# Optimization experiments

Hardware: AMD Instinct MI355X
Metric: run time of the kernel (lower is better)

The kernel has to match this reference:

```python
import jax, jax.numpy as jnp
import numpy as np

DIM = 1024
HEADS = 16
DIM_HEAD = 64
DIM_INNER = HEADS * DIM_HEAD
SCALE = DIM_HEAD ** -0.5


def rmsnorm(x, w):
    eps = jnp.asarray(jnp.finfo(x.dtype).eps, x.dtype)
    var = jnp.mean(jnp.square(x), axis=-1, keepdims=True)
    return x * jax.lax.rsqrt(var + eps) * w


def setup_inputs() -> dict:
    key = jax.random.key(0)
    ks = jax.random.split(key, 6)
    tokens = jax.random.normal(ks[0], (2, 2048, DIM), dtype=jnp.float32)
    norm_w = jnp.ones((DIM,), dtype=jnp.float32)
    Wq = jax.random.normal(ks[1], (DIM, DIM_INNER), dtype=jnp.float32) * 0.02
    Wkv = jax.random.normal(ks[2], (DIM, 2 * DIM_INNER), dtype=jnp.float32) * 0.02
    Wout = jax.random.normal(ks[3], (DIM_INNER, DIM), dtype=jnp.float32) * 0.02
    Wg = jax.random.normal(ks[4], (DIM, HEADS), dtype=jnp.float32) * 0.02
    return {"tokens": tokens, "norm_w": norm_w, "Wq": Wq, "Wkv": Wkv, "Wout": Wout, "Wg": Wg}


def reference(tokens, norm_w, Wq, Wkv, Wout, Wg):
    b, n, _ = tokens.shape
    x = rmsnorm(tokens, norm_w)                      # [b, n, dim]
    q = x @ Wq                                       # [b, n, h*d]
    kv = x @ Wkv                                     # self-attention: context = tokens
    k, v = jnp.split(kv, 2, axis=-1)

    def split_heads(t):
        return t.reshape(b, n, HEADS, DIM_HEAD).transpose(0, 2, 1, 3)  # [b, h, n, d]

    q, k, v = map(split_heads, (q, k, v))

    sim = jnp.einsum('bhid,bhjd->bhij', q, k) * SCALE  # [b, h, n, n]
    causal_mask = jnp.triu(jnp.ones((n, n), dtype=bool), k=1)
    sim = jnp.where(causal_mask, jnp.asarray(-jnp.finfo(sim.dtype).max, sim.dtype), sim)
    attn = jax.nn.softmax(sim, axis=-1)
    out = jnp.einsum('bhij,bhjd->bhid', attn, v)       # [b, h, n, d]

    gates = jax.nn.sigmoid(x @ Wg)                     # [b, n, h]
    gates = gates.transpose(0, 2, 1)[..., None]        # [b, h, n, 1]
    out = gates * out

    out = out.transpose(0, 2, 1, 3).reshape(b, n, DIM_INNER)  # merge heads
    return out @ Wout                                  # [b, n, dim]
```

## Files before the change

kernel.cpp:

```cpp
#include <hip/hip_runtime.h>
#include <hip/hip_bf16.h>
#include <math.h>

constexpr int BB = 2;
constexpr int NN = 2048;
constexpr int DM = 1024;
constexpr int NH = 16;
constexpr int HD = 64;
constexpr int DI = NH * HD;
constexpr int MT = BB * NN;
constexpr float SM_SCALE = 0.125f * 1.44269504089f;

typedef __attribute__((ext_vector_type(8))) short short8v;
typedef __attribute__((ext_vector_type(4))) float f32x4;

__device__ inline unsigned cvt_pk_bf16(float lo, float hi) {
  unsigned r;
  asm("v_cvt_pk_bf16_f32 %0, %1, %2" : "=v"(r) : "v"(lo), "v"(hi));
  return r;
}
__device__ inline void pl32_swap(unsigned& a, unsigned& b) {
  asm("v_permlane32_swap_b32 %0, %1" : "+v"(a), "+v"(b));
}
__device__ inline void pl16_swap(unsigned& a, unsigned& b) {
  asm("v_permlane16_swap_b32 %0, %1" : "+v"(a), "+v"(b));
}
__device__ __forceinline__ void gload16(const void* g, void* l) {
  __builtin_amdgcn_global_load_lds(
      (const __attribute__((address_space(1))) unsigned int*)g,
      (__attribute__((address_space(3))) unsigned int*)l, 16, 0, 0);
}

__global__ __launch_bounds__(256) void k_rmsnorm(const float* __restrict__ tokens,
                                                 const float* __restrict__ w,
                                                 const float* __restrict__ Wg,
                                                 float* __restrict__ x,
                                                 __hip_bfloat16* __restrict__ xb,
                                                 float* __restrict__ g) {
  __shared__ float xs[DM];
  __shared__ float red[4];
  __shared__ float gred[4][16];
  const int tok = blockIdx.x;
  const int t = threadIdx.x;
  float4 v = ((const float4*)(tokens + (size_t)tok * DM))[t];
  float ss = v.x * v.x + v.y * v.y + v.z * v.z + v.w * v.w;
#pragma unroll
  for (int m = 1; m < 64; m <<= 1) ss += __shfl_xor(ss, m, 64);
  if ((t & 63) == 0) red[t >> 6] = ss;
  __syncthreads();
  float tot = red[0] + red[1] + red[2] + red[3];
  float inv = rsqrtf(tot * (1.0f / DM) + 1.1920929e-7f);
  float4 wv = ((const float4*)w)[t];
  float4 o;
  o.x = v.x * inv * wv.x;
  o.y = v.y * inv * wv.y;
  o.z = v.z * inv * wv.z;
  o.w = v.w * inv * wv.w;
  ((float4*)(x + (size_t)tok * DM))[t] = o;
  uint2 pk = make_uint2(cvt_pk_bf16(o.x, o.y), cvt_pk_bf16(o.z, o.w));
  *(uint2*)(xb + (size_t)tok * DM + t * 4) = pk;
  *(float4*)&xs[t * 4] = o;
  __syncthreads();
  const int h = t & 15, seg = t >> 4, wid = t >> 6;
  const float* xp = &xs[seg * 64];
  const float* wp = Wg + (size_t)(seg * 64) * NH + h;
  float s = 0.f;
#pragma unroll 8
  for (int k = 0; k < 64; k++) s = fmaf(xp[k], wp[(size_t)k * NH], s);
  s += __shfl_xor(s, 16);
  s += __shfl_xor(s, 32);
  if ((t & 63) < 16) gred[wid][h] = s;
  __syncthreads();
  if (t < 16) {
    float tot2 = gred[0][t] + gred[1][t] + gred[2][t] + gred[3][t];
    g[(size_t)tok * NH + t] = 1.f / (1.f + __expf(-tot2));
  }
}

__global__ __launch_bounds__(256) void k_wtrans_all(const float* __restrict__ Wq,
                                                    const float* __restrict__ Wkv,
                                                    const float* __restrict__ Wout,
                                                    __hip_bfloat16* __restrict__ Wqkvt,
                                                    __hip_bfloat16* __restrict__ Woutt) {
  const int bx = blockIdx.x;
  const int kb = blockIdx.y * 32;
  const float* W;
  __hip_bfloat16* dst;
  int N, col0, drow0;
  if (bx < 32) {
    W = Wq; N = DI; col0 = bx * 32; dst = Wqkvt; drow0 = col0;
  } else if (bx < 96) {
    W = Wkv; N = 2 * DI; col0 = (bx - 32) * 32; dst = Wqkvt; drow0 = DI + col0;
  } else {
    W = Wout; N = DM; col0 = (bx - 96) * 32; dst = Woutt; drow0 = col0;
  }
  __shared__ float tile[32][33];
  const int t = threadIdx.x;
  const int c = t & 31, r8 = t >> 5;
#pragma unroll
  for (int i = 0; i < 4; i++)
    tile[r8 + i * 8][c] = W[(size_t)(kb + r8 + i * 8) * N + col0 + c];
  __syncthreads();
#pragma unroll
  for (int i = 0; i < 4; i++)
    dst[(size_t)(drow0 + r8 + i * 8) * DM + kb + c] = __float2bfloat16(tile[c][r8 + i * 8]);
}

template <int MODE>
__global__ __launch_bounds__(256) void k_mgemm(const __hip_bfloat16* __restrict__ A,
                                               const __hip_bfloat16* __restrict__ Bt,
                                               float* __restrict__ C,
                                               __hip_bfloat16* __restrict__ OQ,
                                               __hip_bfloat16* __restrict__ OK,
                                               __hip_bfloat16* __restrict__ OV, int Nc) {
  __shared__ __hip_bfloat16 As[128][32];
  __shared__ __hip_bfloat16 Bs[64][32];
  const int t = threadIdx.x, wid = t >> 6, lane = t & 63;
  const int lq = lane & 15, lg = lane >> 4;
  const int wr = wid >> 1, wc = wid & 1;
  const int m0 = blockIdx.y * 128, n0 = blockIdx.x * 64;
  const int srow = lane >> 2, scol = (lane & 3) * 8;

  const __hip_bfloat16* Ag = A + (size_t)(m0 + wid * 32 + srow) * DM + scol;
  const __hip_bfloat16* Bg = Bt + (size_t)(n0 + wid * 16 + srow) * DM + scol;

  f32x4 acc[4][2];
#pragma unroll
  for (int i = 0; i < 4; i++)
#pragma unroll
    for (int j = 0; j < 2; j++) acc[i][j] = (f32x4){0.f, 0.f, 0.f, 0.f};

  for (int k0 = 0; k0 < DM; k0 += 32) {
    __syncthreads();
    gload16(Ag + k0, &As[wid * 32][0]);
    gload16(Ag + 16 * DM + k0, &As[wid * 32 + 16][0]);
    gload16(Bg + k0, &Bs[wid * 16][0]);
    __syncthreads();
    short8v af[4], bf[2];
#pragma unroll
    for (int i = 0; i < 4; i++) af[i] = *(const short8v*)&As[wr * 64 + i * 16 + lq][lg * 8];
#pragma unroll
    for (int j = 0; j < 2; j++) bf[j] = *(const short8v*)&Bs[wc * 32 + j * 16 + lq][lg * 8];
#pragma unroll
    for (int i = 0; i < 4; i++)
#pragma unroll
      for (int j = 0; j < 2; j++)
        acc[i][j] = __builtin_amdgcn_mfma_f32_16x16x32_bf16(af[i], bf[j], acc[i][j], 0, 0, 0);
  }

#pragma unroll
  for (int i = 0; i < 4; i++) {
    const int mb = m0 + wr * 64 + i * 16 + lg * 4;
#pragma unroll
    for (int j = 0; j < 2; j++) {
      const int c = n0 + wc * 32 + j * 16 + lq;
      if (MODE == 0) {
#pragma unroll
        for (int r = 0; r < 4; r++) C[(size_t)(mb + r) * Nc + c] = acc[i][j][r];
      } else {
        const int b = mb >> 11, nl = mb & (NN - 1);
        if (c < DI) {
          const int h = c >> 6, d = c & 63;
          __hip_bfloat16* dst = OQ + ((size_t)(b * NH + h) * NN + nl) * HD + d;
#pragma unroll
          for (int r = 0; r < 4; r++) dst[(size_t)r * HD] = __float2bfloat16(acc[i][j][r]);
        } else if (c < 2 * DI) {
          const int ck = c - DI;
          const int h = ck >> 6, d = ck & 63;
          __hip_bfloat16* dst = OK + ((size_t)(b * NH + h) * NN + nl) * HD + d;
#pragma unroll
          for (int r = 0; r < 4; r++) dst[(size_t)r * HD] = __float2bfloat16(acc[i][j][r]);
        } else {
          const int cd = c - 2 * DI;
          const int h = cd >> 6, d = cd & 63;
          uint2 pk = make_uint2(cvt_pk_bf16(acc[i][j][0], acc[i][j][1]),
                                cvt_pk_bf16(acc[i][j][2], acc[i][j][3]));
          *(uint2*)(OV + ((size_t)(b * NH + h) * HD + d) * NN + nl) = pk;
        }
      }
    }
  }
}

__global__ __launch_bounds__(64) void k_attn_mfma(const __hip_bfloat16* __restrict__ Qb,
                                                  const __hip_bfloat16* __restrict__ Kb,
                                                  const __hip_bfloat16* __restrict__ Vtb,
                                                  const float* __restrict__ gates,
                                                  __hip_bfloat16* __restrict__ aob,
                                                  float* __restrict__ Opart,
                                                  float* __restrict__ mpart,
                                                  float* __restrict__ lpart) {
  const int bid = blockIdx.x;
  const int xcd = bid & 7;
  const int s = bid >> 3;
  const int gq = s / 96;
  const int t = s % 96;
  const int bh = gq * 8 + xcd;
  const int i = t / 3, j = t % 3;
  int grp, kt0, kt1, chunk;
  if (j < 2) {
    grp = 63 - i;
    chunk = j;
    const int nt = (grp >> 1) + 1;
    const int h0 = (nt + 1) >> 1;
    kt0 = chunk ? h0 : 0;
    kt1 = chunk ? nt : h0;
  } else {
    grp = 31 - i;
    chunk = -1;
    kt0 = 0;
    kt1 = (grp >> 1) + 1;
  }
  const int lane = threadIdx.x;
  const int lg = lane >> 4, lq = lane & 15;
  const int q0 = grp * 32;

  const __hip_bfloat16* Qh = Qb + (size_t)bh * NN * HD;
  const __hip_bfloat16* Kh = Kb + (size_t)bh * NN * HD;
  const __hip_bfloat16* Vh = Vtb + (size_t)bh * HD * NN;

  short8v qf0[2], qf1[2];
#pragma unroll
  for (int ks = 0; ks < 2; ks++) {
    qf0[ks] = *(const short8v*)(Qh + (size_t)(q0 + lq) * HD + ks * 32 + lg * 8);
    qf1[ks] = *(const short8v*)(Qh + (size_t)(q0 + 16 + lq) * HD + ks * 32 + lg * 8);
  }

  f32x4 oacc0[4], oacc1[4];
#pragma unroll
  for (int jx = 0; jx < 4; jx++) {
    oacc0[jx] = (f32x4){0.f, 0.f, 0.f, 0.f};
    oacc1[jx] = (f32x4){0.f, 0.f, 0.f, 0.f};
  }
  float m0r = -3.0e38f, l0p = 0.f, m1r = -3.0e38f, l1p = 0.f;

  auto LOADK = [&](short8v (*kf)[2], int kt) {
    const int kvb = kt * 64;
#pragma unroll
    for (int jx = 0; jx < 4; jx++)
#pragma unroll
      for (int ks = 0; ks < 2; ks++)
        kf[jx][ks] = *(const short8v*)(Kh + (size_t)(kvb + jx * 16 + lq) * HD + ks * 32 + lg * 8);
  };
  auto LOADV = [&](short8v (*vf)[2], int kt) {
    const int kvb = kt * 64;
#pragma unroll
    for (int jx = 0; jx < 4; jx++)
#pragma unroll
      for (int ks = 0; ks < 2; ks++)
        vf[jx][ks] = *(const short8v*)(Vh + (size_t)(jx * 16 + lq) * NN + kvb + ks * 32 + lg * 8);
  };

  auto GROUP = [&](const short8v* qf, f32x4* oacc, float& m_run, float& l_part,
                   int q0g, const short8v (*kf)[2], const short8v (*vf)[2], int kt) {
    const int kvb = kt * 64;
    f32x4 sacc[4];
#pragma unroll
    for (int jx = 0; jx < 4; jx++) sacc[jx] = (f32x4){0.f, 0.f, 0.f, 0.f};
#pragma unroll
    for (int jx = 0; jx < 4; jx++)
#pragma unroll
      for (int ks = 0; ks < 2; ks++)
        sacc[jx] = __builtin_amdgcn_mfma_f32_16x16x32_bf16(kf[jx][ks], qf[ks], sacc[jx], 0, 0, 0);

    const int qg = q0g + lq;
    const bool diag = (kvb + 63 > q0g);
    float ss[4][4];
#pragma unroll
    for (int jx = 0; jx < 4; jx++)
#pragma unroll
      for (int r = 0; r < 4; r++) {
        float v = sacc[jx][r] * SM_SCALE;
        if (diag && (kvb + jx * 16 + lg * 4 + r > qg)) v = -3.0e38f;
        ss[jx][r] = v;
      }

    float tmax = -3.0e38f;
#pragma unroll
    for (int jx = 0; jx < 4; jx++)
#pragma unroll
      for (int r = 0; r < 4; r++) tmax = fmaxf(tmax, ss[jx][r]);

    if (!__all(tmax <= m_run + 8.0f)) {
      float tr = fmaxf(tmax, __shfl_xor(tmax, 16));
      tr = fmaxf(tr, __shfl_xor(tr, 32));
      const float mnew = fmaxf(m_run, tr);
      const float cf = exp2f(m_run - mnew);
      l_part *= cf;
#pragma unroll
      for (int jx = 0; jx < 4; jx++)
#pragma unroll
        for (int r = 0; r < 4; r++) oacc[jx][r] *= cf;
      m_run = mnew;
    }

    float psum = 0.f;
    unsigned upk[4], vpk[4];
#pragma unroll
    for (int jx = 0; jx < 4; jx++) {
      float p0 = exp2f(ss[jx][0] - m_run), p1 = exp2f(ss[jx][1] - m_run);
      float p2 = exp2f(ss[jx][2] - m_run), p3 = exp2f(ss[jx][3] - m_run);
      psum += (p0 + p1) + (p2 + p3);
      upk[jx] = cvt_pk_bf16(p0, p1);
      vpk[jx] = cvt_pk_bf16(p2, p3);
    }
    l_part += psum;

#pragma unroll
    for (int ks = 0; ks < 2; ks++) {
      unsigned w0 = upk[2 * ks], w2 = upk[2 * ks + 1];
      unsigned w1 = vpk[2 * ks], w3 = vpk[2 * ks + 1];
      pl32_swap(w0, w2);
      pl16_swap(w0, w2);
      pl32_swap(w1, w3);
      pl16_swap(w1, w3);
      int4 bw = make_int4((int)w0, (int)w1, (int)w2, (int)w3);
      short8v pb = __builtin_bit_cast(short8v, bw);
#pragma unroll
      for (int jx = 0; jx < 4; jx++)
        oacc[jx] = __builtin_amdgcn_mfma_f32_16x16x32_bf16(vf[jx][ks], pb, oacc[jx], 0, 0, 0);
    }
  };

  short8v kf[4][2], vf[4][2];
  for (int kt = kt0; kt < kt1; kt++) {
    LOADK(kf, kt);
    LOADV(vf, kt);
    GROUP(qf0, oacc0, m0r, l0p, q0, kf, vf, kt);
    GROUP(qf1, oacc1, m1r, l1p, q0 + 16, kf, vf, kt);
  }

  float l0 = l0p + __shfl_xor(l0p, 16);
  l0 += __shfl_xor(l0, 32);
  float l1 = l1p + __shfl_xor(l1p, 16);
  l1 += __shfl_xor(l1, 32);

  if (chunk >= 0) {
    const int gi = grp - 32;
    const size_t pidx = (size_t)(bh * 32 + gi) * 2 + chunk;
    float* Op = Opart + pidx * 2048;
#pragma unroll
    for (int jx = 0; jx < 4; jx++) {
      *(f32x4*)(Op + lq * 64 + jx * 16 + lg * 4) = oacc0[jx];
      *(f32x4*)(Op + (16 + lq) * 64 + jx * 16 + lg * 4) = oacc1[jx];
    }
    if (lane < 16) {
      mpart[pidx * 32 + lane] = m0r;
      mpart[pidx * 32 + 16 + lane] = m1r;
      lpart[pidx * 32 + lane] = l0;
      lpart[pidx * 32 + 16 + lane] = l1;
    }
    return;
  }

  const int b = bh >> 4, h = bh & 15;
  const float g0 = gates[((size_t)(b * NN + q0 + lq)) * NH + h];
  const float g1 = gates[((size_t)(b * NN + q0 + 16 + lq)) * NH + h];
  const float sc0 = g0 / l0, sc1 = g1 / l1;
  __shared__ float ots[32][68];
#pragma unroll
  for (int jx = 0; jx < 4; jx++)
#pragma unroll
    for (int r = 0; r < 4; r++) {
      ots[lq][jx * 16 + lg * 4 + r] = oacc0[jx][r] * sc0;
      ots[16 + lq][jx * 16 + lg * 4 + r] = oacc1[jx][r] * sc1;
    }
  __syncthreads();
  const int d0 = (lane & 3) * 16;
#pragma unroll
  for (int rr = 0; rr < 2; rr++) {
    const int rl = rr * 16 + (lane >> 2);
    __hip_bfloat16* aor = aob + ((size_t)(b * NN + q0 + rl)) * DI + h * HD + d0;
#pragma unroll
    for (int u = 0; u < 4; u++) {
      uint2 pk = make_uint2(
          cvt_pk_bf16(ots[rl][d0 + 4 * u + 0], ots[rl][d0 + 4 * u + 1]),
          cvt_pk_bf16(ots[rl][d0 + 4 * u + 2], ots[rl][d0 + 4 * u + 3]));
      *(uint2*)(aor + 4 * u) = pk;
    }
  }
}

__global__ __launch_bounds__(256) void k_attn_combine(const float* __restrict__ Opart,
                                                      const float* __restrict__ mpart,
                                                      const float* __restrict__ lpart,
                                                      const float* __restrict__ gates,
                                                      __hip_bfloat16* __restrict__ aob) {
  const int hg = blockIdx.x;
  const int h = hg >> 5, gi = hg & 31;
  const int grp = 32 + gi;
  const int t = threadIdx.x;
  const int row = t >> 3, dq = (t & 7) * 8;
  const size_t p0 = (size_t)hg * 2, p1 = p0 + 1;
  const float m0 = mpart[p0 * 32 + row], m1 = mpart[p1 * 32 + row];
  const float l0 = lpart[p0 * 32 + row], l1 = lpart[p1 * 32 + row];
  const float M = fmaxf(m0, m1);
  const float a0 = exp2f(m0 - M), a1 = exp2f(m1 - M);
  const float L = a0 * l0 + a1 * l1;
  const int b = h >> 4, hh = h & 15;
  const int grow = grp * 32 + row;
  const float sc = gates[((size_t)(b * NN + grow)) * NH + hh] / L;
  const float* O0 = Opart + p0 * 2048 + row * 64 + dq;
  const float* O1 = Opart + p1 * 2048 + row * 64 + dq;
  unsigned pk[4];
#pragma unroll
  for (int u = 0; u < 4; u++) {
    float x0 = (a0 * O0[2 * u + 0] + a1 * O1[2 * u + 0]) * sc;
    float x1 = (a0 * O0[2 * u + 1] + a1 * O1[2 * u + 1]) * sc;
    pk[u] = cvt_pk_bf16(x0, x1);
  }
  __hip_bfloat16* dst = aob + ((size_t)(b * NN + grow)) * DI + hh * 64 + dq;
  *(uint4*)dst = make_uint4(pk[0], pk[1], pk[2], pk[3]);
}

extern "C" void kernel_launch(void* const* d_in, const int* in_sizes, int n_in,
                              void* d_out, int out_size, void* d_ws, size_t ws_size,
                              hipStream_t stream) {
  const float* tokens = (const float*)d_in[0];
  const float* norm_w = (const float*)d_in[1];
  const float* Wq     = (const float*)d_in[2];
  const float* Wkv    = (const float*)d_in[3];
  const float* Wout   = (const float*)d_in[4];
  const float* Wg     = (const float*)d_in[5];
  float* out = (float*)d_out;

  float* ws = (float*)d_ws;
  float* x  = ws;
  float* gb = x + (size_t)MT * DM;
  __hip_bfloat16* xb    = (__hip_bfloat16*)(gb + (size_t)MT * NH);
  __hip_bfloat16* aob   = xb + (size_t)MT * DM;
  __hip_bfloat16* Qb    = aob + (size_t)MT * DM;
  __hip_bfloat16* Kb    = Qb + (size_t)MT * DI;
  __hip_bfloat16* Vtb   = Kb + (size_t)MT * DI;
  __hip_bfloat16* Wqkvt = Vtb + (size_t)MT * DI;
  __hip_bfloat16* Woutt = Wqkvt + (size_t)3 * DI * DM;
  float* Opart = (float*)(Woutt + (size_t)DM * DI);
  float* mpart = Opart + (size_t)2048 * 2048;
  float* lpart = mpart + (size_t)2048 * 32;

  k_rmsnorm<<<MT, 256, 0, stream>>>(tokens, norm_w, Wg, x, xb, gb);
  k_wtrans_all<<<dim3(128, 32), 256, 0, stream>>>(Wq, Wkv, Wout, Wqkvt, Woutt);
  k_mgemm<3><<<dim3(3 * DI / 64, MT / 128), 256, 0, stream>>>(
      xb, Wqkvt, nullptr, Qb, Kb, Vtb, 3 * DI);
  k_attn_mfma<<<dim3(32 * 96), 64, 0, stream>>>(Qb, Kb, Vtb, gb, aob, Opart, mpart, lpart);
  k_attn_combine<<<dim3(1024), 256, 0, stream>>>(Opart, mpart, lpart, gb, aob);
  k_mgemm<0><<<dim3(DM / 64, MT / 128), 256, 0, stream>>>(
      aob, Woutt, out, nullptr, nullptr, nullptr, DM);
}
```

Measured before the change: 176.3 us.

## Process 64 query rows per attention wave to reuse K/V loads, drop fp32 x write

The attention kernel now handles four 16-row query groups (64 rows) per single-wave block instead of two, so each K/V tile loaded into registers serves twice as many query rows. The grid is halved, split-chunk indexing and the partial-output layout are resized to match, and the combine kernel is adapted to 64-row groups. Separately, the unused fp32 normalized activation write is removed from the rmsnorm kernel. The cost is more registers per wave (extra accumulators and Q fragments) and fewer blocks, which lowers occupancy and parallelism.

```diff
diff --git a/kernel.cpp b/kernel.cpp
--- a/kernel.cpp
+++ b/kernel.cpp
@@ -34,7 +34,6 @@
 __global__ __launch_bounds__(256) void k_rmsnorm(const float* __restrict__ tokens,
                                                  const float* __restrict__ w,
                                                  const float* __restrict__ Wg,
-                                                 float* __restrict__ x,
                                                  __hip_bfloat16* __restrict__ xb,
                                                  float* __restrict__ g) {
   __shared__ float xs[DM];
@@ -56,7 +55,6 @@
   o.y = v.y * inv * wv.y;
   o.z = v.z * inv * wv.z;
   o.w = v.w * inv * wv.w;
-  ((float4*)(x + (size_t)tok * DM))[t] = o;
   uint2 pk = make_uint2(cvt_pk_bf16(o.x, o.y), cvt_pk_bf16(o.z, o.w));
   *(uint2*)(xb + (size_t)tok * DM + t * 4) = pk;
   *(float4*)&xs[t * 4] = o;
@@ -193,46 +191,51 @@
   const int bid = blockIdx.x;
   const int xcd = bid & 7;
   const int s = bid >> 3;
-  const int gq = s / 96;
-  const int t = s % 96;
+  const int gq = s / 48;
+  const int t = s % 48;
   const int bh = gq * 8 + xcd;
   const int i = t / 3, j = t % 3;
   int grp, kt0, kt1, chunk;
   if (j < 2) {
-    grp = 63 - i;
+    grp = 31 - i;
     chunk = j;
-    const int nt = (grp >> 1) + 1;
+    const int nt = grp + 1;
     const int h0 = (nt + 1) >> 1;
     kt0 = chunk ? h0 : 0;
     kt1 = chunk ? nt : h0;
   } else {
-    grp = 31 - i;
+    grp = 15 - i;
     chunk = -1;
     kt0 = 0;
-    kt1 = (grp >> 1) + 1;
+    kt1 = grp + 1;
   }
   const int lane = threadIdx.x;
   const int lg = lane >> 4, lq = lane & 15;
-  const int q0 = grp * 32;
+  const int q0 = grp * 64;
 
   const __hip_bfloat16* Qh = Qb + (size_t)bh * NN * HD;
   const __hip_bfloat16* Kh = Kb + (size_t)bh * NN * HD;
   const __hip_bfloat16* Vh = Vtb + (size_t)bh * HD * NN;
 
-  short8v qf0[2], qf1[2];
+  short8v qf0[2], qf1[2], qf2[2], qf3[2];
 #pragma unroll
   for (int ks = 0; ks < 2; ks++) {
     qf0[ks] = *(const short8v*)(Qh + (size_t)(q0 + lq) * HD + ks * 32 + lg * 8);
     qf1[ks] = *(const short8v*)(Qh + (size_t)(q0 + 16 + lq) * HD + ks * 32 + lg * 8);
-  }
-
-  f32x4 oacc0[4], oacc1[4];
+    qf2[ks] = *(const short8v*)(Qh + (size_t)(q0 + 32 + lq) * HD + ks * 32 + lg * 8);
+    qf3[ks] = *(const short8v*)(Qh + (size_t)(q0 + 48 + lq) * HD + ks * 32 + lg * 8);
+  }
+
+  f32x4 oacc0[4], oacc1[4], oacc2[4], oacc3[4];
 #pragma unroll
   for (int jx = 0; jx < 4; jx++) {
     oacc0[jx] = (f32x4){0.f, 0.f, 0.f, 0.f};
     oacc1[jx] = (f32x4){0.f, 0.f, 0.f, 0.f};
+    oacc2[jx] = (f32x4){0.f, 0.f, 0.f, 0.f};
+    oacc3[jx] = (f32x4){0.f, 0.f, 0.f, 0.f};
   }
   float m0r = -3.0e38f, l0p = 0.f, m1r = -3.0e38f, l1p = 0.f;
+  float m2r = -3.0e38f, l2p = 0.f, m3r = -3.0e38f, l3p = 0.f;
 
   auto LOADK = [&](short8v (*kf)[2], int kt) {
     const int kvb = kt * 64;
@@ -328,27 +331,35 @@
     LOADV(vf, kt);
     GROUP(qf0, oacc0, m0r, l0p, q0, kf, vf, kt);
     GROUP(qf1, oacc1, m1r, l1p, q0 + 16, kf, vf, kt);
-  }
-
-  float l0 = l0p + __shfl_xor(l0p, 16);
-  l0 += __shfl_xor(l0, 32);
-  float l1 = l1p + __shfl_xor(l1p, 16);
-  l1 += __shfl_xor(l1, 32);
+    GROUP(qf2, oacc2, m2r, l2p, q0 + 32, kf, vf, kt);
+    GROUP(qf3, oacc3, m3r, l3p, q0 + 48, kf, vf, kt);
+  }
+
+  float l0 = l0p + __shfl_xor(l0p, 16); l0 += __shfl_xor(l0, 32);
+  float l1 = l1p + __shfl_xor(l1p, 16); l1 += __shfl_xor(l1, 32);
+  float l2 = l2p + __shfl_xor(l2p, 16); l2 += __shfl_xor(l2, 32);
+  float l3 = l3p + __shfl_xor(l3p, 16); l3 += __shfl_xor(l3, 32);
 
   if (chunk >= 0) {
-    const int gi = grp - 32;
-    const size_t pidx = (size_t)(bh * 32 + gi) * 2 + chunk;
-    float* Op = Opart + pidx * 2048;
+    const int gi = grp - 16;
+    const size_t pidx = (size_t)(bh * 16 + gi) * 2 + chunk;
+    float* Op = Opart + pidx * 4096;
 #pragma unroll
     for (int jx = 0; jx < 4; jx++) {
       *(f32x4*)(Op + lq * 64 + jx * 16 + lg * 4) = oacc0[jx];
       *(f32x4*)(Op + (16 + lq) * 64 + jx * 16 + lg * 4) = oacc1[jx];
+      *(f32x4*)(Op + (32 + lq) * 64 + jx * 16 + lg * 4) = oacc2[jx];
+      *(f32x4*)(Op + (48 + lq) * 64 + jx * 16 + lg * 4) = oacc3[jx];
     }
     if (lane < 16) {
-      mpart[pidx * 32 + lane] = m0r;
-      mpart[pidx * 32 + 16 + lane] = m1r;
-      lpart[pidx * 32 + lane] = l0;
-      lpart[pidx * 32 + 16 + lane] = l1;
+      mpart[pidx * 64 + lane] = m0r;
+      mpart[pidx * 64 + 16 + lane] = m1r;
+      mpart[pidx * 64 + 32 + lane] = m2r;
+      mpart[pidx * 64 + 48 + lane] = m3r;
+      lpart[pidx * 64 + lane] = l0;
+      lpart[pidx * 64 + 16 + lane] = l1;
+      lpart[pidx * 64 + 32 + lane] = l2;
+      lpart[pidx * 64 + 48 + lane] = l3;
     }
     return;
   }
@@ -356,19 +367,23 @@
   const int b = bh >> 4, h = bh & 15;
   const float g0 = gates[((size_t)(b * NN + q0 + lq)) * NH + h];
   const float g1 = gates[((size_t)(b * NN + q0 + 16 + lq)) * NH + h];
-  const float sc0 = g0 / l0, sc1 = g1 / l1;
-  __shared__ float ots[32][68];
+  const float g2 = gates[((size_t)(b * NN + q0 + 32 + lq)) * NH + h];
+  const float g3 = gates[((size_t)(b * NN + q0 + 48 + lq)) * NH + h];
+  const float sc0 = g0 / l0, sc1 = g1 / l1, sc2 = g2 / l2, sc3 = g3 / l3;
+  __shared__ float ots[64][68];
 #pragma unroll
   for (int jx = 0; jx < 4; jx++)
 #pragma unroll
     for (int r = 0; r < 4; r++) {
       ots[lq][jx * 16 + lg * 4 + r] = oacc0[jx][r] * sc0;
       ots[16 + lq][jx * 16 + lg * 4 + r] = oacc1[jx][r] * sc1;
+      ots[32 + lq][jx * 16 + lg * 4 + r] = oacc2[jx][r] * sc2;
+      ots[48 + lq][jx * 16 + lg * 4 + r] = oacc3[jx][r] * sc3;
     }
   __syncthreads();
   const int d0 = (lane & 3) * 16;
 #pragma unroll
-  for (int rr = 0; rr < 2; rr++) {
+  for (int rr = 0; rr < 4; rr++) {
     const int rl = rr * 16 + (lane >> 2);
     __hip_bfloat16* aor = aob + ((size_t)(b * NN + q0 + rl)) * DI + h * HD + d0;
 #pragma unroll
@@ -387,30 +402,31 @@
                                                       const float* __restrict__ gates,
                                                       __hip_bfloat16* __restrict__ aob) {
   const int hg = blockIdx.x;
-  const int h = hg >> 5, gi = hg & 31;
-  const int grp = 32 + gi;
+  const int h = hg >> 4, gi = hg & 15;
+  const int grp = 16 + gi;
   const int t = threadIdx.x;
-  const int row = t >> 3, dq = (t & 7) * 8;
+  const int row = t >> 2, d0 = (t & 3) * 16;
   const size_t p0 = (size_t)hg * 2, p1 = p0 + 1;
-  const float m0 = mpart[p0 * 32 + row], m1 = mpart[p1 * 32 + row];
-  const float l0 = lpart[p0 * 32 + row], l1 = lpart[p1 * 32 + row];
+  const float m0 = mpart[p0 * 64 + row], m1 = mpart[p1 * 64 + row];
+  const float l0 = lpart[p0 * 64 + row], l1 = lpart[p1 * 64 + row];
   const float M = fmaxf(m0, m1);
   const float a0 = exp2f(m0 - M), a1 = exp2f(m1 - M);
   const float L = a0 * l0 + a1 * l1;
   const int b = h >> 4, hh = h & 15;
-  const int grow = grp * 32 + row;
+  const int grow = grp * 64 + row;
   const float sc = gates[((size_t)(b * NN + grow)) * NH + hh] / L;
-  const float* O0 = Opart + p0 * 2048 + row * 64 + dq;
-  const float* O1 = Opart + p1 * 2048 + row * 64 + dq;
-  unsigned pk[4];
-#pragma unroll
-  for (int u = 0; u < 4; u++) {
+  const float* O0 = Opart + p0 * 4096 + row * 64 + d0;
+  const float* O1 = Opart + p1 * 4096 + row * 64 + d0;
+  __hip_bfloat16* dst = aob + ((size_t)(b * NN + grow)) * DI + hh * 64 + d0;
+  unsigned pk[8];
+#pragma unroll
+  for (int u = 0; u < 8; u++) {
     float x0 = (a0 * O0[2 * u + 0] + a1 * O1[2 * u + 0]) * sc;
     float x1 = (a0 * O0[2 * u + 1] + a1 * O1[2 * u + 1]) * sc;
     pk[u] = cvt_pk_bf16(x0, x1);
   }
-  __hip_bfloat16* dst = aob + ((size_t)(b * NN + grow)) * DI + hh * 64 + dq;
   *(uint4*)dst = make_uint4(pk[0], pk[1], pk[2], pk[3]);
+  *(uint4*)(dst + 8) = make_uint4(pk[4], pk[5], pk[6], pk[7]);
 }
 
 extern "C" void kernel_launch(void* const* d_in, const int* in_sizes, int n_in,
@@ -425,8 +441,7 @@
   float* out = (float*)d_out;
 
   float* ws = (float*)d_ws;
-  float* x  = ws;
-  float* gb = x + (size_t)MT * DM;
+  float* gb = ws;
   __hip_bfloat16* xb    = (__hip_bfloat16*)(gb + (size_t)MT * NH);
   __hip_bfloat16* aob   = xb + (size_t)MT * DM;
   __hip_bfloat16* Qb    = aob + (size_t)MT * DM;
@@ -435,15 +450,15 @@
   __hip_bfloat16* Wqkvt = Vtb + (size_t)MT * DI;
   __hip_bfloat16* Woutt = Wqkvt + (size_t)3 * DI * DM;
   float* Opart = (float*)(Woutt + (size_t)DM * DI);
-  float* mpart = Opart + (size_t)2048 * 2048;
-  float* lpart = mpart + (size_t)2048 * 32;
-
-  k_rmsnorm<<<MT, 256, 0, stream>>>(tokens, norm_w, Wg, x, xb, gb);
+  float* mpart = Opart + (size_t)1024 * 4096;
+  float* lpart = mpart + (size_t)1024 * 64;
+
+  k_rmsnorm<<<MT, 256, 0, stream>>>(tokens, norm_w, Wg, xb, gb);
   k_wtrans_all<<<dim3(128, 32), 256, 0, stream>>>(Wq, Wkv, Wout, Wqkvt, Woutt);
   k_mgemm<3><<<dim3(3 * DI / 64, MT / 128), 256, 0, stream>>>(
       xb, Wqkvt, nullptr, Qb, Kb, Vtb, 3 * DI);
-  k_attn_mfma<<<dim3(32 * 96), 64, 0, stream>>>(Qb, Kb, Vtb, gb, aob, Opart, mpart, lpart);
-  k_attn_combine<<<dim3(1024), 256, 0, stream>>>(Opart, mpart, lpart, gb, aob);
+  k_attn_mfma<<<dim3(32 * 48), 64, 0, stream>>>(Qb, Kb, Vtb, gb, aob, Opart, mpart, lpart);
+  k_attn_combine<<<dim3(512), 256, 0, stream>>>(Opart, mpart, lpart, gb, aob);
   k_mgemm<0><<<dim3(DM / 64, MT / 128), 256, 0, stream>>>(
       aob, Woutt, out, nullptr, nullptr, nullptr, DM);
 }
```

Result: no change. 179.4 us (+1.7%).

## Merge rmsnorm and weight transpose kernels; double-buffer K fragments in attention

Applied to the files above, without the earlier changes.

Folds the rmsnorm/gate kernel and the weight-transpose kernel into one launch, with blocks split by index, and stops writing the unused fp32 normalized activations. The attention inner loop now ping-pongs two K fragment buffers so the next tile's K loads are issued before the current tile's compute. This is meant to cut launch overhead and redundant global writes and to hide K load latency. The cost is more registers in the attention kernel, which could reduce occupancy.

```diff
diff --git a/kernel.cpp b/kernel.cpp
--- a/kernel.cpp
+++ b/kernel.cpp
@@ -31,79 +31,79 @@
       (__attribute__((address_space(3))) unsigned int*)l, 16, 0, 0);
 }
 
-__global__ __launch_bounds__(256) void k_rmsnorm(const float* __restrict__ tokens,
-                                                 const float* __restrict__ w,
-                                                 const float* __restrict__ Wg,
-                                                 float* __restrict__ x,
-                                                 __hip_bfloat16* __restrict__ xb,
-                                                 float* __restrict__ g) {
-  __shared__ float xs[DM];
-  __shared__ float red[4];
-  __shared__ float gred[4][16];
-  const int tok = blockIdx.x;
+__global__ __launch_bounds__(256) void k_prep(const float* __restrict__ tokens,
+                                              const float* __restrict__ norm_w,
+                                              const float* __restrict__ Wg,
+                                              const float* __restrict__ Wq,
+                                              const float* __restrict__ Wkv,
+                                              const float* __restrict__ Wout,
+                                              __hip_bfloat16* __restrict__ xb,
+                                              float* __restrict__ g,
+                                              __hip_bfloat16* __restrict__ Wqkvt,
+                                              __hip_bfloat16* __restrict__ Woutt) {
+  const int bid = blockIdx.x;
   const int t = threadIdx.x;
-  float4 v = ((const float4*)(tokens + (size_t)tok * DM))[t];
-  float ss = v.x * v.x + v.y * v.y + v.z * v.z + v.w * v.w;
-#pragma unroll
-  for (int m = 1; m < 64; m <<= 1) ss += __shfl_xor(ss, m, 64);
-  if ((t & 63) == 0) red[t >> 6] = ss;
-  __syncthreads();
-  float tot = red[0] + red[1] + red[2] + red[3];
-  float inv = rsqrtf(tot * (1.0f / DM) + 1.1920929e-7f);
-  float4 wv = ((const float4*)w)[t];
-  float4 o;
-  o.x = v.x * inv * wv.x;
-  o.y = v.y * inv * wv.y;
-  o.z = v.z * inv * wv.z;
-  o.w = v.w * inv * wv.w;
-  ((float4*)(x + (size_t)tok * DM))[t] = o;
-  uint2 pk = make_uint2(cvt_pk_bf16(o.x, o.y), cvt_pk_bf16(o.z, o.w));
-  *(uint2*)(xb + (size_t)tok * DM + t * 4) = pk;
-  *(float4*)&xs[t * 4] = o;
-  __syncthreads();
-  const int h = t & 15, seg = t >> 4, wid = t >> 6;
-  const float* xp = &xs[seg * 64];
-  const float* wp = Wg + (size_t)(seg * 64) * NH + h;
-  float s = 0.f;
+  if (bid < MT) {
+    __shared__ float xs[DM];
+    __shared__ float red[4];
+    __shared__ float gred[4][16];
+    const int tok = bid;
+    float4 v = ((const float4*)(tokens + (size_t)tok * DM))[t];
+    float ss = v.x * v.x + v.y * v.y + v.z * v.z + v.w * v.w;
+#pragma unroll
+    for (int m = 1; m < 64; m <<= 1) ss += __shfl_xor(ss, m, 64);
+    if ((t & 63) == 0) red[t >> 6] = ss;
+    __syncthreads();
+    float tot = red[0] + red[1] + red[2] + red[3];
+    float inv = rsqrtf(tot * (1.0f / DM) + 1.1920929e-7f);
+    float4 wv = ((const float4*)norm_w)[t];
+    float4 o;
+    o.x = v.x * inv * wv.x;
+    o.y = v.y * inv * wv.y;
+    o.z = v.z * inv * wv.z;
+    o.w = v.w * inv * wv.w;
+    uint2 pk = make_uint2(cvt_pk_bf16(o.x, o.y), cvt_pk_bf16(o.z, o.w));
+    *(uint2*)(xb + (size_t)tok * DM + t * 4) = pk;
+    *(float4*)&xs[t * 4] = o;
+    __syncthreads();
+    const int h = t & 15, seg = t >> 4, wid = t >> 6;
+    const float* xp = &xs[seg * 64];
+    const float* wp = Wg + (size_t)(seg * 64) * NH + h;
+    float s = 0.f;
 #pragma unroll 8
-  for (int k = 0; k < 64; k++) s = fmaf(xp[k], wp[(size_t)k * NH], s);
-  s += __shfl_xor(s, 16);
-  s += __shfl_xor(s, 32);
-  if ((t & 63) < 16) gred[wid][h] = s;
-  __syncthreads();
-  if (t < 16) {
-    float tot2 = gred[0][t] + gred[1][t] + gred[2][t] + gred[3][t];
-    g[(size_t)tok * NH + t] = 1.f / (1.f + __expf(-tot2));
-  }
-}
-
-__global__ __launch_bounds__(256) void k_wtrans_all(const float* __restrict__ Wq,
-                                                    const float* __restrict__ Wkv,
-                                                    const float* __restrict__ Wout,
-                                                    __hip_bfloat16* __restrict__ Wqkvt,
-                                                    __hip_bfloat16* __restrict__ Woutt) {
-  const int bx = blockIdx.x;
-  const int kb = blockIdx.y * 32;
-  const float* W;
-  __hip_bfloat16* dst;
-  int N, col0, drow0;
-  if (bx < 32) {
-    W = Wq; N = DI; col0 = bx * 32; dst = Wqkvt; drow0 = col0;
-  } else if (bx < 96) {
-    W = Wkv; N = 2 * DI; col0 = (bx - 32) * 32; dst = Wqkvt; drow0 = DI + col0;
+    for (int k = 0; k < 64; k++) s = fmaf(xp[k], wp[(size_t)k * NH], s);
+    s += __shfl_xor(s, 16);
+    s += __shfl_xor(s, 32);
+    if ((t & 63) < 16) gred[wid][h] = s;
+    __syncthreads();
+    if (t < 16) {
+      float tot2 = gred[0][t] + gred[1][t] + gred[2][t] + gred[3][t];
+      g[(size_t)tok * NH + t] = 1.f / (1.f + __expf(-tot2));
+    }
   } else {
-    W = Wout; N = DM; col0 = (bx - 96) * 32; dst = Woutt; drow0 = col0;
-  }
-  __shared__ float tile[32][33];
-  const int t = threadIdx.x;
-  const int c = t & 31, r8 = t >> 5;
-#pragma unroll
-  for (int i = 0; i < 4; i++)
-    tile[r8 + i * 8][c] = W[(size_t)(kb + r8 + i * 8) * N + col0 + c];
-  __syncthreads();
-#pragma unroll
-  for (int i = 0; i < 4; i++)
-    dst[(size_t)(drow0 + r8 + i * 8) * DM + kb + c] = __float2bfloat16(tile[c][r8 + i * 8]);
+    const int wb = bid - MT;
+    const int bx = wb & 127, by = wb >> 7;
+    const int kb = by * 32;
+    const float* W;
+    __hip_bfloat16* dst;
+    int N, col0, drow0;
+    if (bx < 32) {
+      W = Wq; N = DI; col0 = bx * 32; dst = Wqkvt; drow0 = col0;
+    } else if (bx < 96) {
+      W = Wkv; N = 2 * DI; col0 = (bx - 32) * 32; dst = Wqkvt; drow0 = DI + col0;
+    } else {
+      W = Wout; N = DM; col0 = (bx - 96) * 32; dst = Woutt; drow0 = col0;
+    }
+    __shared__ float tile[32][33];
+    const int c = t & 31, r8 = t >> 5;
+#pragma unroll
+    for (int i = 0; i < 4; i++)
+      tile[r8 + i * 8][c] = W[(size_t)(kb + r8 + i * 8) * N + col0 + c];
+    __syncthreads();
+#pragma unroll
+    for (int i = 0; i < 4; i++)
+      dst[(size_t)(drow0 + r8 + i * 8) * DM + kb + c] = __float2bfloat16(tile[c][r8 + i * 8]);
+  }
 }
 
 template <int MODE>
@@ -322,12 +322,20 @@
     }
   };
 
-  short8v kf[4][2], vf[4][2];
-  for (int kt = kt0; kt < kt1; kt++) {
-    LOADK(kf, kt);
+  short8v kfA[4][2], kfB[4][2], vf[4][2];
+  LOADK(kfA, kt0);
+  int kt = kt0;
+  while (true) {
     LOADV(vf, kt);
-    GROUP(qf0, oacc0, m0r, l0p, q0, kf, vf, kt);
-    GROUP(qf1, oacc1, m1r, l1p, q0 + 16, kf, vf, kt);
+    if (kt + 1 < kt1) LOADK(kfB, kt + 1);
+    GROUP(qf0, oacc0, m0r, l0p, q0, kfA, vf, kt);
+    GROUP(qf1, oacc1, m1r, l1p, q0 + 16, kfA, vf, kt);
+    if (++kt == kt1) break;
+    LOADV(vf, kt);
+    if (kt + 1 < kt1) LOADK(kfA, kt + 1);
+    GROUP(qf0, oacc0, m0r, l0p, q0, kfB, vf, kt);
+    GROUP(qf1, oacc1, m1r, l1p, q0 + 16, kfB, vf, kt);
+    if (++kt == kt1) break;
   }
 
   float l0 = l0p + __shfl_xor(l0p, 16);
@@ -425,8 +433,7 @@
   float* out = (float*)d_out;
 
   float* ws = (float*)d_ws;
-  float* x  = ws;
-  float* gb = x + (size_t)MT * DM;
+  float* gb = ws;
   __hip_bfloat16* xb    = (__hip_bfloat16*)(gb + (size_t)MT * NH);
   __hip_bfloat16* aob   = xb + (size_t)MT * DM;
   __hip_bfloat16* Qb    = aob + (size_t)MT * DM;
@@ -438,8 +445,8 @@
   float* mpart = Opart + (size_t)2048 * 2048;
   float* lpart = mpart + (size_t)2048 * 32;
 
-  k_rmsnorm<<<MT, 256, 0, stream>>>(tokens, norm_w, Wg, x, xb, gb);
-  k_wtrans_all<<<dim3(128, 32), 256, 0, stream>>>(Wq, Wkv, Wout, Wqkvt, Woutt);
+  k_prep<<<dim3(MT + 4096), 256, 0, stream>>>(tokens, norm_w, Wg, Wq, Wkv, Wout,
+                                              xb, gb, Wqkvt, Woutt);
   k_mgemm<3><<<dim3(3 * DI / 64, MT / 128), 256, 0, stream>>>(
       xb, Wqkvt, nullptr, Qb, Kb, Vtb, 3 * DI);
   k_attn_mfma<<<dim3(32 * 96), 64, 0, stream>>>(Qb, Kb, Vtb, gb, aob, Opart, mpart, lpart);
```

New measurement: 167.8 us. 1.05x faster.
